# Kernel tuning notes

Hardware: AMD Instinct MI355X
Metric: run time of the kernel (lower is better)

The kernel has to match this reference:

```python
import jax, jax.numpy as jnp
import numpy as np

MODEL_DIM = 1024
NUM_HEADS = 16
HEAD_DIM = MODEL_DIM // NUM_HEADS
B, SQ, SK = 1, 4096, 4096


def setup_inputs() -> dict:
    key = jax.random.key(0)
    ks = jax.random.split(key, 10)
    s = 0.02  # realistic init scale for weights
    inp = {
        "x_query": jax.random.normal(ks[0], (B, SQ, MODEL_DIM), jnp.float32),
        "x_context": jax.random.normal(ks[1], (B, SK, MODEL_DIM), jnp.float32),
        # causal mask [B,1,Sq,Sk]; 0 -> masked
        "mask": jnp.tril(jnp.ones((SQ, SK), jnp.int32))[None, None, :, :],
        "wq": jax.random.normal(ks[2], (MODEL_DIM, MODEL_DIM), jnp.float32) * s,
        "bq": jnp.zeros((MODEL_DIM,), jnp.float32),
        "wk": jax.random.normal(ks[3], (MODEL_DIM, MODEL_DIM), jnp.float32) * s,
        "bk": jnp.zeros((MODEL_DIM,), jnp.float32),
        "wv": jax.random.normal(ks[4], (MODEL_DIM, MODEL_DIM), jnp.float32) * s,
        "bv": jnp.zeros((MODEL_DIM,), jnp.float32),
        "wo": jax.random.normal(ks[5], (MODEL_DIM, MODEL_DIM), jnp.float32) * s,
        "bo": jnp.zeros((MODEL_DIM,), jnp.float32),
    }
    return inp


def reference(x_query, x_context, mask, wq, bq, wk, bk, wv, bv, wo, bo):
    b = x_query.shape[0]
    # torch nn.Linear: y = x @ W.T + b
    q = x_query @ wq.T + bq
    k = x_context @ wk.T + bk
    v = x_context @ wv.T + bv
    # [B, S, D] -> [B, H, S, Hd]
    def split_heads(t):
        return t.reshape(b, -1, NUM_HEADS, HEAD_DIM).transpose(0, 2, 1, 3)
    q, k, v = split_heads(q), split_heads(k), split_heads(v)
    scale = 1.0 / jnp.sqrt(jnp.asarray(HEAD_DIM, q.dtype))
    scores = jnp.einsum('bhqd,bhkd->bhqk', q, k) * scale  # [B,H,Sq,Sk]
    scores = jnp.where(mask == 0, jnp.asarray(-1e9, scores.dtype), scores)
    attn = jax.nn.softmax(scores, axis=-1)
    # dropout: eval mode (identity)
    ctx = jnp.einsum('bhqk,bhkd->bhqd', attn, v)
    ctx = ctx.transpose(0, 2, 1, 3).reshape(b, -1, MODEL_DIM)
    return ctx @ wo.T + bo
```

## Files before the change

kernel.cpp:

```cpp
#include <hip/hip_runtime.h>

typedef __bf16 bf16x8 __attribute__((ext_vector_type(8)));
typedef float f32x4 __attribute__((ext_vector_type(4)));
typedef float f32x16 __attribute__((ext_vector_type(16)));
typedef unsigned int u32x2v __attribute__((ext_vector_type(2)));

#define GLD16(gp, lp) __builtin_amdgcn_global_load_lds( \
    (const __attribute__((address_space(1))) void*)(gp), \
    (__attribute__((address_space(3))) void*)(lp), 16, 0, 0)

__device__ __forceinline__ unsigned short f2bf(float f) {
  unsigned int u = __float_as_uint(f);
  u += 0x7FFFu + ((u >> 16) & 1u);
  return (unsigned short)(u >> 16);
}

__device__ __forceinline__ unsigned int cvtpk(float lo, float hi) {
  unsigned int r;
  asm("v_cvt_pk_bf16_f32 %0, %1, %2" : "=v"(r) : "v"(lo), "v"(hi));
  return r;
}

__device__ __forceinline__ float exp2f_(float x) {
#if __has_builtin(__builtin_amdgcn_exp2f)
  return __builtin_amdgcn_exp2f(x);
#else
  float r; asm("v_exp_f32 %0, %1" : "=v"(r) : "v"(x)); return r;
#endif
}

__device__ __forceinline__ u32x2v pswap(unsigned int a, unsigned int b) {
#if __has_builtin(__builtin_amdgcn_permlane32_swap)
  u32x2v r;
  auto q = __builtin_amdgcn_permlane32_swap(a, b, false, false);
  r[0] = q[0]; r[1] = q[1];
  return r;
#else
  unsigned int pa = (unsigned int)__shfl_xor((int)a, 32);
  unsigned int pb = (unsigned int)__shfl_xor((int)b, 32);
  int hi = (threadIdx.x >> 5) & 1;
  u32x2v r;
  r[0] = hi ? pb : a;
  r[1] = hi ? b : pa;
  return r;
#endif
}

__global__ __launch_bounds__(256) void cast6(
    const float* __restrict__ xq, const float* __restrict__ xc,
    const float* __restrict__ wq, const float* __restrict__ wk,
    const float* __restrict__ wv, const float* __restrict__ wo,
    unsigned short* __restrict__ d) {
  int i = (blockIdx.x * 256 + threadIdx.x) * 4;
  const float* s; int off;
  if      (i < (4 << 20))  { s = xq; off = 0; }
  else if (i < (8 << 20))  { s = xc; off = 4 << 20; }
  else if (i < (9 << 20))  { s = wq; off = 8 << 20; }
  else if (i < (10 << 20)) { s = wk; off = 9 << 20; }
  else if (i < (11 << 20)) { s = wv; off = 10 << 20; }
  else                     { s = wo; off = 11 << 20; }
  float4 v = *(const float4*)(s + (i - off));
  ushort4 o;
  o.x = f2bf(v.x); o.y = f2bf(v.y); o.z = f2bf(v.z); o.w = f2bf(v.w);
  *(ushort4*)(d + i) = o;
}

template<int OUTF32>
__device__ __forceinline__ void gemm_body(
    const unsigned short* __restrict__ A, const unsigned short* __restrict__ B,
    const float* __restrict__ bias, void* __restrict__ C,
    int N, int K, int bm, int bn, float scale,
    unsigned short* As, unsigned short* Bs) {
  const int t = threadIdx.x;
  const int lane = t & 63, wid = t >> 6;
  const int wm = wid >> 1, wn = wid & 1;
  const int l15 = lane & 15, l4 = lane >> 4, l7 = lane & 7;

  f32x4 acc[2][4];
#pragma unroll
  for (int i = 0; i < 2; ++i)
#pragma unroll
    for (int j = 0; j < 4; ++j) acc[i][j] = (f32x4){0.f, 0.f, 0.f, 0.f};

  const char* Ab = (const char*)A;
  const char* Bb = (const char*)B;
  const int ldb = K * 2;

  for (int kt = 0; kt < K; kt += 64) {
#pragma unroll
    for (int c = 0; c < 2; ++c) {
      int id = c * 512 + t;
      int row = id >> 3;
      int ch = (id & 7) ^ (row & 7);
      const char* ga = Ab + (size_t)(bm * 128 + row) * ldb + kt * 2 + ch * 16;
      GLD16(ga, (char*)As + id * 16);
      const char* gb = Bb + (size_t)(bn * 128 + row) * ldb + kt * 2 + ch * 16;
      GLD16(gb, (char*)Bs + id * 16);
    }
    __syncthreads();
#pragma unroll
    for (int kk = 0; kk < 2; ++kk) {
      bf16x8 af[2], bfr[4];
#pragma unroll
      for (int mi = 0; mi < 2; ++mi) {
        int row = wm * 32 + mi * 16 + l15;
        int ch = (l4 + 4 * kk) ^ l7;
        af[mi] = *(const bf16x8*)((const char*)As + row * 128 + ch * 16);
      }
#pragma unroll
      for (int ni = 0; ni < 4; ++ni) {
        int row = wn * 64 + ni * 16 + l15;
        int ch = (l4 + 4 * kk) ^ l7;
        bfr[ni] = *(const bf16x8*)((const char*)Bs + row * 128 + ch * 16);
      }
#pragma unroll
      for (int mi = 0; mi < 2; ++mi)
#pragma unroll
        for (int ni = 0; ni < 4; ++ni)
          acc[mi][ni] = __builtin_amdgcn_mfma_f32_16x16x32_bf16(
              af[mi], bfr[ni], acc[mi][ni], 0, 0, 0);
    }
    __syncthreads();
  }

#pragma unroll
  for (int ni = 0; ni < 4; ++ni) {
    int col = bn * 128 + wn * 64 + ni * 16 + l15;
    float bv = bias[col];
#pragma unroll
    for (int mi = 0; mi < 2; ++mi) {
#pragma unroll
      for (int r = 0; r < 4; ++r) {
        int row = bm * 128 + wm * 32 + mi * 16 + l4 * 4 + r;
        float v = (acc[mi][ni][r] + bv) * scale;
        if (OUTF32) ((float*)C)[(size_t)row * N + col] = v;
        else ((unsigned short*)C)[(size_t)row * N + col] = f2bf(v);
      }
    }
  }
}

__global__ __launch_bounds__(512) void gemm_qkv(
    const unsigned short* __restrict__ xq, const unsigned short* __restrict__ xc,
    const unsigned short* __restrict__ wq, const unsigned short* __restrict__ wk,
    const unsigned short* __restrict__ wv,
    const float* __restrict__ bq, const float* __restrict__ bk,
    const float* __restrict__ bv,
    unsigned short* __restrict__ Qo, unsigned short* __restrict__ Ko,
    unsigned short* __restrict__ Vo) {
  __shared__ __align__(16) unsigned short As[128 * 64];
  __shared__ __align__(16) unsigned short Bs[128 * 64];
  const unsigned short* A; const unsigned short* B; const float* bias;
  unsigned short* C; float scale;
  if (blockIdx.z == 0)      { A = xq; B = wq; bias = bq; C = Qo; scale = 0.18033688011112042f; }
  else if (blockIdx.z == 1) { A = xc; B = wk; bias = bk; C = Ko; scale = 1.0f; }
  else                      { A = xc; B = wv; bias = bv; C = Vo; scale = 1.0f; }
  gemm_body<0>(A, B, bias, (void*)C, 1024, 1024, blockIdx.y, blockIdx.x, scale, As, Bs);
}

__global__ __launch_bounds__(512) void gemm_out(
    const unsigned short* __restrict__ A, const unsigned short* __restrict__ B,
    const float* __restrict__ bias, float* __restrict__ C) {
  __shared__ __align__(16) unsigned short As[128 * 64];
  __shared__ __align__(16) unsigned short Bs[128 * 64];
  gemm_body<1>(A, B, bias, (void*)C, 1024, 1024, blockIdx.y, blockIdx.x, 1.0f, As, Bs);
}

__global__ __launch_bounds__(256)
void flash_attn(
    const unsigned short* __restrict__ Q, const unsigned short* __restrict__ K,
    const unsigned short* __restrict__ V, unsigned short* __restrict__ O,
    unsigned short* __restrict__ partO, float* __restrict__ lBase) {
  __shared__ __align__(16) char smem[24576];

  const int b = blockIdx.x;
  const int h = b & 15;
  const int ep = b >> 4;
  int qb, role, P;
  if (ep < 32)      { qb = 31 - (ep >> 2); role = ep & 3; P = 4; }
  else if (ep < 56) { int k = ep - 32; qb = 23 - k / 3; role = k % 3; P = 3; }
  else if (ep < 72) { int k = ep - 56; qb = 15 - (k >> 1); role = k & 1; P = 2; }
  else              { qb = 7 - (ep - 72); role = 0; P = 1; }

  const int T = 2 * qb + 2;
  const int t0 = (role * T) / P;
  const int n  = ((role + 1) * T) / P - t0;

  const int t = threadIdx.x;
  const int lane = t & 63, w = t >> 6;
  const int l31 = lane & 31, hi = lane >> 5;
  const int q0w = qb * 128 + w * 32;
  const int qwmax = q0w + 31;

  bf16x8 qf[4];
#pragma unroll
  for (int ks = 0; ks < 4; ++ks)
    qf[ks] = *(const bf16x8*)(Q + (size_t)(q0w + l31) * 1024 + h * 64 + ks * 16 + hi * 8);

  f32x16 po0, po1;
#pragma unroll
  for (int r = 0; r < 16; ++r) { po0[r] = 0.f; po1[r] = 0.f; }
  float lacc[8];
#pragma unroll
  for (int i = 0; i < 8; ++i) lacc[i] = 0.f;

  const int vd4 = (t & 15) * 4;
  const int vkvr = (t >> 4) * 4;
  uint2 va[4];

  auto stageK = [&](int tile, int buf) {
#pragma unroll
    for (int i = 0; i < 2; ++i) {
      int id = i * 256 + t;
      int row = id >> 3;
      int ch = (id & 7) ^ (row & 7);
      GLD16((const char*)K + (size_t)(tile * 64 + row) * 2048 + h * 128 + ch * 16,
            smem + buf * 8192 + id * 16);
    }
  };
  auto loadV = [&](int tile) {
#pragma unroll
    for (int i = 0; i < 4; ++i)
      va[i] = *(const uint2*)(V + (size_t)(tile * 64 + vkvr + i) * 1024 + h * 64 + vd4);
  };
  auto writeV = [&]() {
    char* Vt = smem + 16384;
#pragma unroll
    for (int j = 0; j < 4; ++j) {
      unsigned sel = (j & 1) ? 0x07060302u : 0x05040100u;
      unsigned s01 = (j < 2) ? __builtin_amdgcn_perm(va[1].x, va[0].x, sel)
                             : __builtin_amdgcn_perm(va[1].y, va[0].y, sel);
      unsigned s23 = (j < 2) ? __builtin_amdgcn_perm(va[3].x, va[2].x, sel)
                             : __builtin_amdgcn_perm(va[3].y, va[2].y, sel);
      int row = vd4 + j;
      int sw = (vkvr * 2) ^ (((row >> 2) & 7) << 4);
      *(uint2*)(Vt + row * 128 + sw) = make_uint2(s01, s23);
    }
  };

  stageK(t0, 0);
  loadV(t0);
  writeV();
  __syncthreads();

  for (int it = 0; it < n; ++it) {
    const int c = it & 1;
    const bool pf = (it + 1) < n;
    if (pf) { stageK(t0 + it + 1, c ^ 1); loadV(t0 + it + 1); }

    const int kv0 = (t0 + it) * 64;
    if (kv0 <= qwmax) {
      const char* Ks = smem + c * 8192;
      const char* Vt = smem + 16384;
      f32x16 s0, s1;
#pragma unroll
      for (int r = 0; r < 16; ++r) { s0[r] = 0.f; s1[r] = 0.f; }
      __builtin_amdgcn_s_setprio(1);
#pragma unroll
      for (int ks = 0; ks < 4; ++ks) {
        int c0 = ((ks * 2 + hi) ^ (l31 & 7)) << 4;
        bf16x8 k0 = *(const bf16x8*)(Ks + l31 * 128 + c0);
        bf16x8 k1 = *(const bf16x8*)(Ks + (32 + l31) * 128 + c0);
        s0 = __builtin_amdgcn_mfma_f32_32x32x16_bf16(k0, qf[ks], s0, 0, 0, 0);
        s1 = __builtin_amdgcn_mfma_f32_32x32x16_bf16(k1, qf[ks], s1, 0, 0, 0);
      }
      __builtin_amdgcn_s_setprio(0);
      if (kv0 + 63 > q0w) {
        int q = q0w + l31;
#pragma unroll
        for (int r = 0; r < 16; ++r) {
          int kvi = kv0 + (r & 3) + 8 * (r >> 2) + 4 * hi;
          if (kvi > q) s0[r] = -1e30f;
          if (kvi + 32 > q) s1[r] = -1e30f;
        }
      }
#pragma unroll
      for (int r = 0; r < 16; ++r) s0[r] = exp2f_(s0[r]);
#pragma unroll
      for (int r = 0; r < 16; ++r) s1[r] = exp2f_(s1[r]);
#pragma unroll
      for (int i = 0; i < 8; ++i)
        lacc[i] += (s0[2 * i] + s0[2 * i + 1]) + (s1[2 * i] + s1[2 * i + 1]);

#pragma unroll
      for (int kp = 0; kp < 4; ++kp) {
        const f32x16& sv = (kp < 2) ? s0 : s1;
        const int bb = (kp & 1) * 8;
        unsigned c0v = cvtpk(sv[bb + 0], sv[bb + 1]);
        unsigned c1v = cvtpk(sv[bb + 2], sv[bb + 3]);
        unsigned c2v = cvtpk(sv[bb + 4], sv[bb + 5]);
        unsigned c3v = cvtpk(sv[bb + 6], sv[bb + 7]);
        u32x2v w02 = pswap(c0v, c2v);
        u32x2v w13 = pswap(c1v, c3v);
        union { unsigned u[4]; bf16x8 v; } pfr;
        pfr.u[0] = w02[0]; pfr.u[1] = w13[0]; pfr.u[2] = w02[1]; pfr.u[3] = w13[1];
        int cb = kp * 2 + hi;
        __builtin_amdgcn_s_setprio(1);
        {
          int row = l31;
          bf16x8 vf = *(const bf16x8*)(Vt + row * 128 + ((cb ^ ((row >> 2) & 7)) << 4));
          po0 = __builtin_amdgcn_mfma_f32_32x32x16_bf16(vf, pfr.v, po0, 0, 0, 0);
        }
        {
          int row = 32 + l31;
          bf16x8 vf = *(const bf16x8*)(Vt + row * 128 + ((cb ^ ((row >> 2) & 7)) << 4));
          po1 = __builtin_amdgcn_mfma_f32_32x32x16_bf16(vf, pfr.v, po1, 0, 0, 0);
        }
        __builtin_amdgcn_s_setprio(0);
      }
    }
    __syncthreads();
    if (pf) writeV();
    __syncthreads();
  }

  float l4v[4];
#pragma unroll
  for (int i = 0; i < 4; ++i) l4v[i] = lacc[i] + lacc[4 + i];
  float ps = (l4v[0] + l4v[1]) + (l4v[2] + l4v[3]);
  u32x2v sw2 = pswap(__float_as_uint(ps), __float_as_uint(ps));
  const float l_i = __uint_as_float(sw2[0]) + __uint_as_float(sw2[1]);
  const float rinv = 1.0f / l_i;

  if (P > 1) {
    const int slot = h * 72 + ep;
    unsigned u[16];
#pragma unroll
    for (int i = 0; i < 8; ++i) u[i] = cvtpk(po0[2 * i] * rinv, po0[2 * i + 1] * rinv);
#pragma unroll
    for (int i = 0; i < 8; ++i) u[8 + i] = cvtpk(po1[2 * i] * rinv, po1[2 * i + 1] * rinv);
    char* bO = (char*)partO + (size_t)slot * 16384 + t * 64;
    *(uint4*)(bO +  0) = make_uint4(u[0], u[1], u[2], u[3]);
    *(uint4*)(bO + 16) = make_uint4(u[4], u[5], u[6], u[7]);
    *(uint4*)(bO + 32) = make_uint4(u[8], u[9], u[10], u[11]);
    *(uint4*)(bO + 48) = make_uint4(u[12], u[13], u[14], u[15]);
    if (!hi) {
      lBase[(size_t)slot * 128 + w * 32 + l31] = l_i;
    }
    return;
  }

  {
    int qlocal = w * 32 + l31;
#pragma unroll
    for (int g = 0; g < 4; ++g) {
#pragma unroll
      for (int db = 0; db < 2; ++db) {
        const f32x16& p = db ? po1 : po0;
        unsigned w0 = cvtpk(p[g * 4 + 0] * rinv, p[g * 4 + 1] * rinv);
        unsigned w1 = cvtpk(p[g * 4 + 2] * rinv, p[g * 4 + 3] * rinv);
        int d0 = db * 32 + 8 * g + 4 * hi;
        int byte = qlocal * 128 + ((d0 * 2) ^ ((qlocal & 7) << 4));
        *(uint2*)(smem + byte) = make_uint2(w0, w1);
      }
    }
  }
  __syncthreads();
#pragma unroll
  for (int it = 0; it < 4; ++it) {
    int r = it * 32 + (t >> 3);
    int c = t & 7;
    uint4 val = *(const uint4*)(smem + r * 128 + ((c ^ (r & 7)) << 4));
    *(uint4*)((char*)O + (size_t)(qb * 128 + r) * 2048 + h * 128 + c * 16) = val;
  }
}

__global__ __launch_bounds__(256) void flash_merge(
    const unsigned short* __restrict__ partO, const float* __restrict__ lBase,
    unsigned short* __restrict__ O) {
  const int p = blockIdx.x;
  const int h = p & 15;
  const int j = p >> 4;
  int qb, P, e0;
  if (j < 8)       { qb = 31 - j; P = 4; e0 = j * 4; }
  else if (j < 16) { qb = 23 - (j - 8); P = 3; e0 = 32 + (j - 8) * 3; }
  else             { qb = 15 - (j - 16); P = 2; e0 = 56 + (j - 16) * 2; }
  const int t = threadIdx.x;
  const int s = t >> 6, hi = (t >> 5) & 1, l31 = t & 31;

  float acc[32];
#pragma unroll
  for (int i = 0; i < 32; ++i) acc[i] = 0.f;
  float den = 0.f;
#pragma unroll
  for (int r = 0; r < 4; ++r) {
    if (r < P) {
      float wgt = lBase[(size_t)(h * 72 + e0 + r) * 128 + s * 32 + l31];
      den += wgt;
      const uint4* bO = (const uint4*)((const char*)partO +
                         (size_t)(h * 72 + e0 + r) * 16384 + t * 64);
      uint4 a = bO[0], b2 = bO[1], c2 = bO[2], d2 = bO[3];
      unsigned uu[16] = {a.x, a.y, a.z, a.w, b2.x, b2.y, b2.z, b2.w,
                         c2.x, c2.y, c2.z, c2.w, d2.x, d2.y, d2.z, d2.w};
#pragma unroll
      for (int i = 0; i < 16; ++i) {
        acc[2 * i]     += wgt * __uint_as_float(uu[i] << 16);
        acc[2 * i + 1] += wgt * __uint_as_float(uu[i] & 0xFFFF0000u);
      }
    }
  }
  float rinv = 1.0f / den;
  const int q = qb * 128 + s * 32 + l31;
  unsigned short* orow = O + (size_t)q * 1024 + h * 64;
#pragma unroll
  for (int r = 0; r < 16; ++r) {
    int d = (r & 3) + 8 * (r >> 2) + 4 * hi;
    orow[d]      = f2bf(acc[r] * rinv);
    orow[d + 32] = f2bf(acc[16 + r] * rinv);
  }
}

extern "C" void kernel_launch(void* const* d_in, const int* in_sizes, int n_in,
                              void* d_out, int out_size, void* d_ws, size_t ws_size,
                              hipStream_t stream) {
  const float* xq = (const float*)d_in[0];
  const float* xc = (const float*)d_in[1];
  const float* wq = (const float*)d_in[3];
  const float* bq = (const float*)d_in[4];
  const float* wk = (const float*)d_in[5];
  const float* bk = (const float*)d_in[6];
  const float* wv = (const float*)d_in[7];
  const float* bv = (const float*)d_in[8];
  const float* wo = (const float*)d_in[9];
  const float* bo = (const float*)d_in[10];

  unsigned short* wsb = (unsigned short*)d_ws;
  unsigned short* xqb = wsb;
  unsigned short* xcb = wsb + (4 << 20);
  unsigned short* wqb = wsb + (8 << 20);
  unsigned short* wkb = wsb + (9 << 20);
  unsigned short* wvb = wsb + (10 << 20);
  unsigned short* wob = wsb + (11 << 20);
  unsigned short* Qb  = wsb + (12 << 20);
  unsigned short* Kb  = wsb + (16 << 20);
  unsigned short* Vb  = wsb + (20 << 20);
  unsigned short* Cb  = wsb + (24 << 20);

  unsigned short* partO = (unsigned short*)d_ws;
  float* lBase = (float*)((char*)d_ws + (18u << 20));

  cast6<<<12288, 256, 0, stream>>>(xq, xc, wq, wk, wv, wo, wsb);

  dim3 gq(1024 / 128, 4096 / 128, 3);
  gemm_qkv<<<gq, 512, 0, stream>>>(xqb, xcb, wqb, wkb, wvb, bq, bk, bv, Qb, Kb, Vb);

  flash_attn<<<1280, 256, 0, stream>>>(Qb, Kb, Vb, Cb, partO, lBase);

  flash_merge<<<384, 256, 0, stream>>>(partO, lBase, Cb);

  dim3 go(1024 / 128, 4096 / 128);
  gemm_out<<<go, 512, 0, stream>>>(Cb, wob, bo, (float*)d_out);
}
```

Measured before the change: 152.9 us.

## Fuse activation cast into QKV GEMM, double-buffer V, rebalance attention split, retile output GEMM

The QKV GEMM now reads fp32 activations directly and converts them to bf16 while staging into shared memory, so the cast kernel only handles the weights and a full pass over the activations is dropped. Flash attention double-buffers the transposed V tile, which removes one barrier per iteration at the cost of more shared memory. The split-K partition is rebalanced to at most 3 partitions with fewer blocks, which shrinks merge traffic. The output GEMM switches to 64x128 tiles to launch more blocks. The fp32 A loads bypass the async global-to-LDS path and may stall the QKV GEMM.

```diff
diff --git a/kernel.cpp b/kernel.cpp
--- a/kernel.cpp
+++ b/kernel.cpp
@@ -46,28 +46,25 @@
 #endif
 }
 
-__global__ __launch_bounds__(256) void cast6(
-    const float* __restrict__ xq, const float* __restrict__ xc,
+__global__ __launch_bounds__(256) void cast_w(
     const float* __restrict__ wq, const float* __restrict__ wk,
     const float* __restrict__ wv, const float* __restrict__ wo,
     unsigned short* __restrict__ d) {
   int i = (blockIdx.x * 256 + threadIdx.x) * 4;
   const float* s; int off;
-  if      (i < (4 << 20))  { s = xq; off = 0; }
-  else if (i < (8 << 20))  { s = xc; off = 4 << 20; }
-  else if (i < (9 << 20))  { s = wq; off = 8 << 20; }
-  else if (i < (10 << 20)) { s = wk; off = 9 << 20; }
-  else if (i < (11 << 20)) { s = wv; off = 10 << 20; }
-  else                     { s = wo; off = 11 << 20; }
+  if      (i < (1 << 20)) { s = wq; off = 0; }
+  else if (i < (2 << 20)) { s = wk; off = 1 << 20; }
+  else if (i < (3 << 20)) { s = wv; off = 2 << 20; }
+  else                    { s = wo; off = 3 << 20; }
   float4 v = *(const float4*)(s + (i - off));
   ushort4 o;
   o.x = f2bf(v.x); o.y = f2bf(v.y); o.z = f2bf(v.z); o.w = f2bf(v.w);
   *(ushort4*)(d + i) = o;
 }
 
-template<int OUTF32>
+template<int OUTF32, int AF32>
 __device__ __forceinline__ void gemm_body(
-    const unsigned short* __restrict__ A, const unsigned short* __restrict__ B,
+    const void* __restrict__ Av, const unsigned short* __restrict__ B,
     const float* __restrict__ bias, void* __restrict__ C,
     int N, int K, int bm, int bn, float scale,
     unsigned short* As, unsigned short* Bs) {
@@ -82,7 +79,6 @@
 #pragma unroll
     for (int j = 0; j < 4; ++j) acc[i][j] = (f32x4){0.f, 0.f, 0.f, 0.f};
 
-  const char* Ab = (const char*)A;
   const char* Bb = (const char*)B;
   const int ldb = K * 2;
 
@@ -92,10 +88,32 @@
       int id = c * 512 + t;
       int row = id >> 3;
       int ch = (id & 7) ^ (row & 7);
-      const char* ga = Ab + (size_t)(bm * 128 + row) * ldb + kt * 2 + ch * 16;
-      GLD16(ga, (char*)As + id * 16);
       const char* gb = Bb + (size_t)(bn * 128 + row) * ldb + kt * 2 + ch * 16;
       GLD16(gb, (char*)Bs + id * 16);
+    }
+    if (AF32) {
+      const float* Af = (const float*)Av;
+#pragma unroll
+      for (int c = 0; c < 2; ++c) {
+        int id = c * 512 + t;
+        int row = id >> 3, cc = id & 7;
+        const float4* src = (const float4*)(Af + (size_t)(bm * 128 + row) * K + kt + cc * 8);
+        float4 v0 = src[0], v1 = src[1];
+        uint4 u;
+        u.x = cvtpk(v0.x, v0.y); u.y = cvtpk(v0.z, v0.w);
+        u.z = cvtpk(v1.x, v1.y); u.w = cvtpk(v1.z, v1.w);
+        *(uint4*)((char*)As + (row * 8 + (cc ^ (row & 7))) * 16) = u;
+      }
+    } else {
+      const char* Ab = (const char*)Av;
+#pragma unroll
+      for (int c = 0; c < 2; ++c) {
+        int id = c * 512 + t;
+        int row = id >> 3;
+        int ch = (id & 7) ^ (row & 7);
+        const char* ga = Ab + (size_t)(bm * 128 + row) * ldb + kt * 2 + ch * 16;
+        GLD16(ga, (char*)As + id * 16);
+      }
     }
     __syncthreads();
 #pragma unroll
@@ -141,7 +159,7 @@
 }
 
 __global__ __launch_bounds__(512) void gemm_qkv(
-    const unsigned short* __restrict__ xq, const unsigned short* __restrict__ xc,
+    const float* __restrict__ xq, const float* __restrict__ xc,
     const unsigned short* __restrict__ wq, const unsigned short* __restrict__ wk,
     const unsigned short* __restrict__ wv,
     const float* __restrict__ bq, const float* __restrict__ bk,
@@ -150,20 +168,90 @@
     unsigned short* __restrict__ Vo) {
   __shared__ __align__(16) unsigned short As[128 * 64];
   __shared__ __align__(16) unsigned short Bs[128 * 64];
-  const unsigned short* A; const unsigned short* B; const float* bias;
+  const float* A; const unsigned short* B; const float* bias;
   unsigned short* C; float scale;
   if (blockIdx.z == 0)      { A = xq; B = wq; bias = bq; C = Qo; scale = 0.18033688011112042f; }
   else if (blockIdx.z == 1) { A = xc; B = wk; bias = bk; C = Ko; scale = 1.0f; }
   else                      { A = xc; B = wv; bias = bv; C = Vo; scale = 1.0f; }
-  gemm_body<0>(A, B, bias, (void*)C, 1024, 1024, blockIdx.y, blockIdx.x, scale, As, Bs);
+  gemm_body<0, 1>(A, B, bias, (void*)C, 1024, 1024, blockIdx.y, blockIdx.x, scale, As, Bs);
 }
 
 __global__ __launch_bounds__(512) void gemm_out(
     const unsigned short* __restrict__ A, const unsigned short* __restrict__ B,
     const float* __restrict__ bias, float* __restrict__ C) {
-  __shared__ __align__(16) unsigned short As[128 * 64];
+  __shared__ __align__(16) unsigned short As[64 * 64];
   __shared__ __align__(16) unsigned short Bs[128 * 64];
-  gemm_body<1>(A, B, bias, (void*)C, 1024, 1024, blockIdx.y, blockIdx.x, 1.0f, As, Bs);
+  const int bn = blockIdx.x, bm = blockIdx.y;
+  const int t = threadIdx.x;
+  const int lane = t & 63, wid = t >> 6;
+  const int wm = wid >> 2, wn = wid & 3;
+  const int l15 = lane & 15, l4 = lane >> 4, l7 = lane & 7;
+
+  f32x4 acc[2][2];
+#pragma unroll
+  for (int i = 0; i < 2; ++i)
+#pragma unroll
+    for (int j = 0; j < 2; ++j) acc[i][j] = (f32x4){0.f, 0.f, 0.f, 0.f};
+
+  const char* Ab = (const char*)A;
+  const char* Bb = (const char*)B;
+  const int ldb = 2048;
+
+  for (int kt = 0; kt < 1024; kt += 64) {
+    {
+      int id = t;
+      int row = id >> 3;
+      int ch = (id & 7) ^ (row & 7);
+      const char* ga = Ab + (size_t)(bm * 64 + row) * ldb + kt * 2 + ch * 16;
+      GLD16(ga, (char*)As + id * 16);
+    }
+#pragma unroll
+    for (int c = 0; c < 2; ++c) {
+      int id = c * 512 + t;
+      int row = id >> 3;
+      int ch = (id & 7) ^ (row & 7);
+      const char* gb = Bb + (size_t)(bn * 128 + row) * ldb + kt * 2 + ch * 16;
+      GLD16(gb, (char*)Bs + id * 16);
+    }
+    __syncthreads();
+#pragma unroll
+    for (int kk = 0; kk < 2; ++kk) {
+      bf16x8 af[2], bfr[2];
+#pragma unroll
+      for (int mi = 0; mi < 2; ++mi) {
+        int row = wm * 32 + mi * 16 + l15;
+        int ch = (l4 + 4 * kk) ^ l7;
+        af[mi] = *(const bf16x8*)((const char*)As + row * 128 + ch * 16);
+      }
+#pragma unroll
+      for (int ni = 0; ni < 2; ++ni) {
+        int row = wn * 32 + ni * 16 + l15;
+        int ch = (l4 + 4 * kk) ^ l7;
+        bfr[ni] = *(const bf16x8*)((const char*)Bs + row * 128 + ch * 16);
+      }
+#pragma unroll
+      for (int mi = 0; mi < 2; ++mi)
+#pragma unroll
+        for (int ni = 0; ni < 2; ++ni)
+          acc[mi][ni] = __builtin_amdgcn_mfma_f32_16x16x32_bf16(
+              af[mi], bfr[ni], acc[mi][ni], 0, 0, 0);
+    }
+    __syncthreads();
+  }
+
+#pragma unroll
+  for (int ni = 0; ni < 2; ++ni) {
+    int col = bn * 128 + wn * 32 + ni * 16 + l15;
+    float bv = bias[col];
+#pragma unroll
+    for (int mi = 0; mi < 2; ++mi) {
+#pragma unroll
+      for (int r = 0; r < 4; ++r) {
+        int row = bm * 64 + wm * 32 + mi * 16 + l4 * 4 + r;
+        C[(size_t)row * 1024 + col] = acc[mi][ni][r] + bv;
+      }
+    }
+  }
 }
 
 __global__ __launch_bounds__(256)
@@ -171,16 +259,15 @@
     const unsigned short* __restrict__ Q, const unsigned short* __restrict__ K,
     const unsigned short* __restrict__ V, unsigned short* __restrict__ O,
     unsigned short* __restrict__ partO, float* __restrict__ lBase) {
-  __shared__ __align__(16) char smem[24576];
+  __shared__ __align__(16) char smem[32768];
 
   const int b = blockIdx.x;
   const int h = b & 15;
   const int ep = b >> 4;
   int qb, role, P;
-  if (ep < 32)      { qb = 31 - (ep >> 2); role = ep & 3; P = 4; }
-  else if (ep < 56) { int k = ep - 32; qb = 23 - k / 3; role = k % 3; P = 3; }
-  else if (ep < 72) { int k = ep - 56; qb = 15 - (k >> 1); role = k & 1; P = 2; }
-  else              { qb = 7 - (ep - 72); role = 0; P = 1; }
+  if (ep < 30)      { qb = 31 - ep / 3; role = ep % 3; P = 3; }
+  else if (ep < 52) { int k = ep - 30; qb = 21 - (k >> 1); role = k & 1; P = 2; }
+  else              { qb = 10 - (ep - 52); role = 0; P = 1; }
 
   const int T = 2 * qb + 2;
   const int t0 = (role * T) / P;
@@ -223,8 +310,8 @@
     for (int i = 0; i < 4; ++i)
       va[i] = *(const uint2*)(V + (size_t)(tile * 64 + vkvr + i) * 1024 + h * 64 + vd4);
   };
-  auto writeV = [&]() {
-    char* Vt = smem + 16384;
+  auto writeV = [&](int buf) {
+    char* Vt = smem + 16384 + buf * 8192;
 #pragma unroll
     for (int j = 0; j < 4; ++j) {
       unsigned sel = (j & 1) ? 0x07060302u : 0x05040100u;
@@ -240,7 +327,7 @@
 
   stageK(t0, 0);
   loadV(t0);
-  writeV();
+  writeV(0);
   __syncthreads();
 
   for (int it = 0; it < n; ++it) {
@@ -251,7 +338,7 @@
     const int kv0 = (t0 + it) * 64;
     if (kv0 <= qwmax) {
       const char* Ks = smem + c * 8192;
-      const char* Vt = smem + 16384;
+      const char* Vt = smem + 16384 + c * 8192;
       f32x16 s0, s1;
 #pragma unroll
       for (int r = 0; r < 16; ++r) { s0[r] = 0.f; s1[r] = 0.f; }
@@ -309,8 +396,7 @@
         __builtin_amdgcn_s_setprio(0);
       }
     }
-    __syncthreads();
-    if (pf) writeV();
+    if (pf) writeV(c ^ 1);
     __syncthreads();
   }
 
@@ -323,7 +409,7 @@
   const float rinv = 1.0f / l_i;
 
   if (P > 1) {
-    const int slot = h * 72 + ep;
+    const int slot = h * 52 + ep;
     unsigned u[16];
 #pragma unroll
     for (int i = 0; i < 8; ++i) u[i] = cvtpk(po0[2 * i] * rinv, po0[2 * i + 1] * rinv);
@@ -372,9 +458,8 @@
   const int h = p & 15;
   const int j = p >> 4;
   int qb, P, e0;
-  if (j < 8)       { qb = 31 - j; P = 4; e0 = j * 4; }
-  else if (j < 16) { qb = 23 - (j - 8); P = 3; e0 = 32 + (j - 8) * 3; }
-  else             { qb = 15 - (j - 16); P = 2; e0 = 56 + (j - 16) * 2; }
+  if (j < 10) { qb = 31 - j; P = 3; e0 = j * 3; }
+  else        { qb = 21 - (j - 10); P = 2; e0 = 30 + (j - 10) * 2; }
   const int t = threadIdx.x;
   const int s = t >> 6, hi = (t >> 5) & 1, l31 = t & 31;
 
@@ -383,12 +468,12 @@
   for (int i = 0; i < 32; ++i) acc[i] = 0.f;
   float den = 0.f;
 #pragma unroll
-  for (int r = 0; r < 4; ++r) {
+  for (int r = 0; r < 3; ++r) {
     if (r < P) {
-      float wgt = lBase[(size_t)(h * 72 + e0 + r) * 128 + s * 32 + l31];
+      float wgt = lBase[(size_t)(h * 52 + e0 + r) * 128 + s * 32 + l31];
       den += wgt;
       const uint4* bO = (const uint4*)((const char*)partO +
-                         (size_t)(h * 72 + e0 + r) * 16384 + t * 64);
+                         (size_t)(h * 52 + e0 + r) * 16384 + t * 64);
       uint4 a = bO[0], b2 = bO[1], c2 = bO[2], d2 = bO[3];
       unsigned uu[16] = {a.x, a.y, a.z, a.w, b2.x, b2.y, b2.z, b2.w,
                          c2.x, c2.y, c2.z, c2.w, d2.x, d2.y, d2.z, d2.w};
@@ -425,8 +510,6 @@
   const float* bo = (const float*)d_in[10];
 
   unsigned short* wsb = (unsigned short*)d_ws;
-  unsigned short* xqb = wsb;
-  unsigned short* xcb = wsb + (4 << 20);
   unsigned short* wqb = wsb + (8 << 20);
   unsigned short* wkb = wsb + (9 << 20);
   unsigned short* wvb = wsb + (10 << 20);
@@ -437,17 +520,17 @@
   unsigned short* Cb  = wsb + (24 << 20);
 
   unsigned short* partO = (unsigned short*)d_ws;
-  float* lBase = (float*)((char*)d_ws + (18u << 20));
-
-  cast6<<<12288, 256, 0, stream>>>(xq, xc, wq, wk, wv, wo, wsb);
+  float* lBase = (float*)((char*)d_ws + (14u << 20));
+
+  cast_w<<<4096, 256, 0, stream>>>(wq, wk, wv, wo, wqb);
 
   dim3 gq(1024 / 128, 4096 / 128, 3);
-  gemm_qkv<<<gq, 512, 0, stream>>>(xqb, xcb, wqb, wkb, wvb, bq, bk, bv, Qb, Kb, Vb);
-
-  flash_attn<<<1280, 256, 0, stream>>>(Qb, Kb, Vb, Cb, partO, lBase);
-
-  flash_merge<<<384, 256, 0, stream>>>(partO, lBase, Cb);
-
-  dim3 go(1024 / 128, 4096 / 128);
+  gemm_qkv<<<gq, 512, 0, stream>>>(xq, xc, wqb, wkb, wvb, bq, bk, bv, Qb, Kb, Vb);
+
+  flash_attn<<<1008, 256, 0, stream>>>(Qb, Kb, Vb, Cb, partO, lBase);
+
+  flash_merge<<<336, 256, 0, stream>>>(partO, lBase, Cb);
+
+  dim3 go(1024 / 128, 4096 / 64);
   gemm_out<<<go, 512, 0, stream>>>(Cb, wob, bo, (float*)d_out);
 }
```

Result: slower. 159.3 us (+4.2%).
